# Performance work log

Hardware: AMD Instinct MI355X
Metric: run time of the kernel (lower is better)

## Reference

```python
import jax, jax.numpy as jnp
import numpy as np

N_TASKS = 32
D = 2097152  # flattened gradient dim
MAX_ITER = 250
STOP_CRIT = 1e-6
EPS = 1e-8


def setup_inputs() -> dict:
    key = jax.random.key(0)
    vecs = jax.random.normal(key, (N_TASKS, D), dtype=jnp.float32)
    return {"vecs": vecs}


def _line_solver(v11, v12, v22):
    # min-norm point on the segment between two vectors (vectorized / scalar)
    g = (v22 - v12) / (v11 + v22 - 2.0 * v12 + EPS)
    c = v22 + g * (v12 - v22)
    gamma = jnp.where(v12 >= v22, 0.0, g)
    gamma = jnp.where(v12 >= v11, 1.0, gamma)
    cost = jnp.where(v12 >= v22, v22, c)
    cost = jnp.where(v12 >= v11, v11, cost)
    return gamma, cost


def _planar_init(G, n):
    iu_np, ju_np = np.triu_indices(n, 1)
    iu = jnp.asarray(iu_np)
    ju = jnp.asarray(ju_np)
    vivj = G[iu, ju]
    vivi = G[iu, iu]
    vjvj = G[ju, ju]
    gamma, cost = _line_solver(vivi, vivj, vjvj)
    off = jnp.argmin(cost)
    sol = jnp.zeros(n, dtype=G.dtype)
    sol = sol.at[iu[off]].set(gamma[off]).at[ju[off]].set(1.0 - gamma[off])
    return sol


def _proj_simplex(gamma, i_grid):
    s = jnp.sort(gamma)[::-1]  # descending
    tmp_max = (jnp.cumsum(s) - 1.0) / i_grid
    cond = tmp_max[:-1] > s[1:]
    first = jnp.argmax(cond)  # index of first True (0 if none)
    tmax = jnp.where(jnp.any(cond), tmp_max[:-1][first], tmp_max[-1])
    return jnp.maximum(gamma - tmax, 0.0)


def _next_point(cur, grad, n, i_grid):
    proj = grad - jnp.sum(grad) / n
    neg = proj < 0
    pos = proj > 0
    tm1 = jnp.where(neg, -cur / jnp.where(neg, proj, 1.0), jnp.inf)
    tm2 = jnp.where(pos, (1.0 - cur) / jnp.where(pos, proj, 1.0), jnp.inf)
    m1 = jnp.min(jnp.where(tm1 > 1e-7, tm1, jnp.inf))
    t = jnp.where(jnp.isfinite(m1), m1, 1.0)
    m2 = jnp.min(jnp.where(tm2 > 1e-7, tm2, jnp.inf))
    t = jnp.minimum(t, m2)  # no-op if m2 is inf
    nxt = proj * t + cur
    return _proj_simplex(nxt, i_grid)


def reference(vecs):
    n = vecs.shape[0]
    G = vecs @ vecs.T  # [n, n] grammian; only memory-heavy step
    sol0 = _planar_init(G, n)
    i_grid = jnp.arange(n, dtype=G.dtype) + 1.0
    n_f = jnp.asarray(n, dtype=G.dtype)

    def body(carry, _):
        sol, done = carry
        grad_dir = -(G @ sol)
        newp = _next_point(sol, grad_dir, n_f, i_grid)
        Gs = G @ sol
        Gn = G @ newp
        v11 = sol @ Gs
        v12 = sol @ Gn
        v22 = newp @ Gn
        gamma, _ = _line_solver(v11, v12, v22)
        new_sol = gamma * sol + (1.0 - gamma) * newp
        stop = jnp.sum(jnp.abs(new_sol - sol)) < STOP_CRIT
        nd = done | stop
        # original returns the OLD sol_vec when change < stop_crit
        out = jnp.where(nd, sol, new_sol)
        return (out, nd), None

    (sol, _), _ = jax.lax.scan(body, (sol0, jnp.array(False)), None, length=MAX_ITER)
    return sol
```

## Files before the change

kernel.cpp:

```cpp
#include <hip/hip_runtime.h>

#define NT 32
#define EPSF 1e-8f

#define TILE_COLS 64
#define COL_PITCH 36
#define GR_THREADS 256
#define WAVES_PB 4
#define TILES_PW 16

__global__ __launch_bounds__(GR_THREADS, 2)
void gram_kernel(const float* __restrict__ vecs, double* __restrict__ Gd, int D)
{
    __shared__ float tile[WAVES_PB][TILE_COLS * COL_PITCH];
    __shared__ float Gpart[NT * NT];

    const int tid  = threadIdx.x;
    const int wave = tid >> 6;
    const int lane = tid & 63;

    for (int e = tid; e < NT * NT; e += GR_THREADS) Gpart[e] = 0.0f;
    __syncthreads();

    const int cj = lane >> 4;
    const int p  = lane & 15;
    const int pi = p >> 2;
    const int pk = p & 3;

    const int lrow = lane >> 4;
    const int lcol = (lane & 15) << 2;

    float acc[8][8];
#pragma unroll
    for (int r = 0; r < 8; r++)
#pragma unroll
        for (int c = 0; c < 8; c++) acc[r][c] = 0.0f;

    float* my = tile[wave];
    const long colbase0 = (long)blockIdx.x * (WAVES_PB * TILES_PW * TILE_COLS)
                        + (long)wave * (TILES_PW * TILE_COLS);

    float4 pre[8];
#pragma unroll
    for (int rr = 0; rr < 8; rr++) {
        const int row = (rr << 2) + lrow;
        pre[rr] = *(const float4*)(vecs + (long)row * D + colbase0 + lcol);
    }

    for (int t = 0; t < TILES_PW; t++) {
        __threadfence_block();
#pragma unroll
        for (int rr = 0; rr < 8; rr++) {
            const int row = (rr << 2) + lrow;
            my[(lcol + 0) * COL_PITCH + row] = pre[rr].x;
            my[(lcol + 1) * COL_PITCH + row] = pre[rr].y;
            my[(lcol + 2) * COL_PITCH + row] = pre[rr].z;
            my[(lcol + 3) * COL_PITCH + row] = pre[rr].w;
        }
        __threadfence_block();
        if (t + 1 < TILES_PW) {
            const long cb = colbase0 + (long)(t + 1) * TILE_COLS;
#pragma unroll
            for (int rr = 0; rr < 8; rr++) {
                const int row = (rr << 2) + lrow;
                pre[rr] = *(const float4*)(vecs + (long)row * D + cb + lcol);
            }
        }
#pragma unroll
        for (int jt = 0; jt < 16; jt++) {
            const int j = (jt << 2) + cj;
            const float* col = my + j * COL_PITCH;
            const float4 a0 = *(const float4*)(col + 8 * pi);
            const float4 a1 = *(const float4*)(col + 8 * pi + 4);
            const float4 b0 = *(const float4*)(col + 8 * pk);
            const float4 b1 = *(const float4*)(col + 8 * pk + 4);
            const float a[8] = {a0.x, a0.y, a0.z, a0.w, a1.x, a1.y, a1.z, a1.w};
            const float b[8] = {b0.x, b0.y, b0.z, b0.w, b1.x, b1.y, b1.z, b1.w};
#pragma unroll
            for (int r = 0; r < 8; r++)
#pragma unroll
                for (int c = 0; c < 8; c++)
                    acc[r][c] = fmaf(a[r], b[c], acc[r][c]);
        }
    }

#pragma unroll
    for (int r = 0; r < 8; r++)
#pragma unroll
        for (int c = 0; c < 8; c++) {
            float v = acc[r][c];
            v += __shfl_xor(v, 16);
            v += __shfl_xor(v, 32);
            if (lane < 16)
                atomicAdd(&Gpart[(8 * pi + r) * NT + (8 * pk + c)], v);
        }
    __syncthreads();
    for (int e = tid; e < NT * NT; e += GR_THREADS)
        atomicAdd(&Gd[e], (double)Gpart[e]);
}

__device__ __forceinline__ float bsum32(float v) {
#pragma unroll
    for (int m = 1; m < 32; m <<= 1) v += __shfl_xor(v, m);
    return v;
}
__device__ __forceinline__ float bmin32(float v) {
#pragma unroll
    for (int m = 1; m < 32; m <<= 1) v = fminf(v, __shfl_xor(v, m));
    return v;
}

__global__ __launch_bounds__(64)
void solver_kernel(const double* __restrict__ Gd, float* __restrict__ out)
{
    __shared__ float Gsh[NT * 33];
    const int lane = threadIdx.x;

    for (int t2 = 0; t2 < 16; t2++) {
        int e = t2 * 64 + lane;
        Gsh[(e >> 5) * 33 + (e & 31)] = (float)Gd[e];
    }
    __syncthreads();

    float Grow[NT];
#pragma unroll
    for (int k = 0; k < NT; k++)
        Grow[k] = (lane < NT) ? Gsh[lane * 33 + k] : 0.0f;

    float bestCost = INFINITY, bestGamma = 0.0f;
    int bestEnc = 0x7FFFFFFF;
    for (int a = 0; a < NT - 1; a++) {
        int b = a + 1 + lane;
        if (b < NT) {
            float v11 = Gsh[a * 33 + a];
            float v12 = Gsh[a * 33 + b];
            float v22 = Gsh[b * 33 + b];
            float g = (v22 - v12) / (v11 + v22 - 2.0f * v12 + EPSF);
            float c = v22 + g * (v12 - v22);
            float gamma = (v12 >= v22) ? 0.0f : g;
            float cost  = (v12 >= v22) ? v22 : c;
            if (v12 >= v11) { gamma = 1.0f; cost = v11; }
            int enc = a * NT + b;
            if (cost < bestCost) { bestCost = cost; bestEnc = enc; bestGamma = gamma; }
        }
    }
#pragma unroll
    for (int m = 1; m < 64; m <<= 1) {
        float oc = __shfl_xor(bestCost, m);
        int   oe = __shfl_xor(bestEnc, m);
        float og = __shfl_xor(bestGamma, m);
        if (oc < bestCost || (oc == bestCost && oe < bestEnc)) {
            bestCost = oc; bestEnc = oe; bestGamma = og;
        }
    }
    const int bi = bestEnc >> 5, bj = bestEnc & 31;

    float sol = 0.0f;
    if (lane == bi) sol = bestGamma;
    if (lane == bj) sol = 1.0f - bestGamma;

    for (int it = 0; it < 250; it++) {
        float s0 = 0, s1 = 0, s2 = 0, s3 = 0;
#pragma unroll
        for (int k = 0; k < NT; k += 4) {
            s0 = fmaf(Grow[k + 0], __shfl(sol, k + 0), s0);
            s1 = fmaf(Grow[k + 1], __shfl(sol, k + 1), s1);
            s2 = fmaf(Grow[k + 2], __shfl(sol, k + 2), s2);
            s3 = fmaf(Grow[k + 3], __shfl(sol, k + 3), s3);
        }
        float Gsol = (s0 + s1) + (s2 + s3);

        float grad = -Gsol;
        float proj = grad - bsum32(grad) * 0.03125f;

        float tm1 = (proj < 0.0f) ? (-sol / proj) : INFINITY;
        float tm2 = (proj > 0.0f) ? ((1.0f - sol) / proj) : INFINITY;
        float m1 = bmin32((tm1 > 1e-7f) ? tm1 : INFINITY);
        float m2 = bmin32((tm2 > 1e-7f) ? tm2 : INFINITY);
        float t = __builtin_isinf(m1) ? 1.0f : m1;
        t = fminf(t, m2);
        float nxt = fmaf(proj, t, sol);

        float s = nxt;
#pragma unroll
        for (int k = 2; k <= 32; k <<= 1)
#pragma unroll
            for (int j = k >> 1; j >= 1; j >>= 1) {
                float pp = __shfl_xor(s, j);
                bool descSeg = (lane & k) == 0;
                bool lower = (lane & j) == 0;
                float mn = fminf(s, pp), mx = fmaxf(s, pp);
                s = (descSeg == lower) ? mx : mn;
            }
        float cs = s;
#pragma unroll
        for (int d = 1; d < 32; d <<= 1) {
            float pp = __shfl_up(cs, d, 32);
            if ((lane & 31) >= d) cs += pp;
        }
        float tmpm = (cs - 1.0f) / (float)((lane & 31) + 1);
        float snext = __shfl_down(s, 1, 32);
        bool cond = ((lane & 31) < 31) && (tmpm > snext);
        unsigned long long bal = __ballot(cond ? 1 : 0) & 0x7FFFFFFFull;
        float tmax;
        if (bal != 0ULL) {
            int first = __builtin_ctzll(bal);
            tmax = __shfl(tmpm, first);
        } else {
            tmax = __shfl(tmpm, 31);
        }
        float newp = fmaxf(nxt - tmax, 0.0f);
        if (lane >= NT) newp = 0.0f;

        float n0 = 0, n1 = 0, n2 = 0, n3 = 0;
#pragma unroll
        for (int k = 0; k < NT; k += 4) {
            n0 = fmaf(Grow[k + 0], __shfl(newp, k + 0), n0);
            n1 = fmaf(Grow[k + 1], __shfl(newp, k + 1), n1);
            n2 = fmaf(Grow[k + 2], __shfl(newp, k + 2), n2);
            n3 = fmaf(Grow[k + 3], __shfl(newp, k + 3), n3);
        }
        float Gn = (n0 + n1) + (n2 + n3);

        float v11 = bsum32(sol * Gsol);
        float v12 = bsum32(sol * Gn);
        float v22 = bsum32(newp * Gn);

        float g = (v22 - v12) / (v11 + v22 - 2.0f * v12 + EPSF);
        float gamma = (v12 >= v22) ? 0.0f : g;
        gamma = (v12 >= v11) ? 1.0f : gamma;

        float new_sol = gamma * sol + (1.0f - gamma) * newp;
        float diff = bsum32(fabsf(new_sol - sol));
        diff = __shfl(diff, 0);
        if (diff < 1e-6f) break;
        sol = new_sol;
    }
    if (lane < NT) out[lane] = sol;
}

extern "C" void kernel_launch(void* const* d_in, const int* in_sizes, int n_in,
                              void* d_out, int out_size, void* d_ws, size_t ws_size,
                              hipStream_t stream) {
    const float* vecs = (const float*)d_in[0];
    float* out = (float*)d_out;
    double* Gd = (double*)d_ws;
    const int D = in_sizes[0] / NT;

    hipMemsetAsync(Gd, 0, NT * NT * sizeof(double), stream);

    const int cols_per_block = WAVES_PB * TILES_PW * TILE_COLS;
    const int grid = D / cols_per_block;
    gram_kernel<<<grid, GR_THREADS, 0, stream>>>(vecs, Gd, D);
    solver_kernel<<<1, 64, 0, stream>>>(Gd, out);
}
```

Before: 430.1 us.

## Swizzle Gram tile layout, halve tiles per wave, use DPP/readlane in solver

The Gram kernel now loads one column per lane with scalar loads and stores rows into an XOR-swizzled 32-wide shared tile instead of a padded transpose. Tiles per wave drop to 8 and the occupancy hint rises to 4 blocks per CU, doubling the grid. The serial solver swaps ds_bpermute-based shuffles for DPP row ops, ds_swizzle and readlane to shorten the per-iteration latency chain. The risks are more register pressure from the 32-float prefetch array, scalar global loads that may coalesce worse, and subtle cross-row DPP correctness in the scans.

```diff
diff --git a/kernel.cpp b/kernel.cpp
--- a/kernel.cpp
+++ b/kernel.cpp
@@ -4,15 +4,14 @@
 #define EPSF 1e-8f
 
 #define TILE_COLS 64
-#define COL_PITCH 36
 #define GR_THREADS 256
 #define WAVES_PB 4
-#define TILES_PW 16
-
-__global__ __launch_bounds__(GR_THREADS, 2)
+#define TILES_PW 8
+
+__global__ __launch_bounds__(GR_THREADS, 4)
 void gram_kernel(const float* __restrict__ vecs, double* __restrict__ Gd, int D)
 {
-    __shared__ float tile[WAVES_PB][TILE_COLS * COL_PITCH];
+    __shared__ __align__(16) float tile[WAVES_PB][TILE_COLS * 32];
     __shared__ float Gpart[NT * NT];
 
     const int tid  = threadIdx.x;
@@ -22,13 +21,12 @@
     for (int e = tid; e < NT * NT; e += GR_THREADS) Gpart[e] = 0.0f;
     __syncthreads();
 
+    float* my = tile[wave];
+    const int swz = lane & 7;
+
     const int cj = lane >> 4;
-    const int p  = lane & 15;
-    const int pi = p >> 2;
-    const int pk = p & 3;
-
-    const int lrow = lane >> 4;
-    const int lcol = (lane & 15) << 2;
+    const int pi = (lane >> 2) & 3;
+    const int pk = lane & 3;
 
     float acc[8][8];
 #pragma unroll
@@ -36,44 +34,34 @@
 #pragma unroll
         for (int c = 0; c < 8; c++) acc[r][c] = 0.0f;
 
-    float* my = tile[wave];
-    const long colbase0 = (long)blockIdx.x * (WAVES_PB * TILES_PW * TILE_COLS)
-                        + (long)wave * (TILES_PW * TILE_COLS);
-
-    float4 pre[8];
-#pragma unroll
-    for (int rr = 0; rr < 8; rr++) {
-        const int row = (rr << 2) + lrow;
-        pre[rr] = *(const float4*)(vecs + (long)row * D + colbase0 + lcol);
-    }
+    const long base0 = (long)blockIdx.x * (WAVES_PB * TILES_PW * TILE_COLS)
+                     + (long)wave * (TILES_PW * TILE_COLS) + lane;
+
+    float pre[32];
+#pragma unroll
+    for (int r = 0; r < 32; r++) pre[r] = vecs[(long)r * D + base0];
 
     for (int t = 0; t < TILES_PW; t++) {
-        __threadfence_block();
-#pragma unroll
-        for (int rr = 0; rr < 8; rr++) {
-            const int row = (rr << 2) + lrow;
-            my[(lcol + 0) * COL_PITCH + row] = pre[rr].x;
-            my[(lcol + 1) * COL_PITCH + row] = pre[rr].y;
-            my[(lcol + 2) * COL_PITCH + row] = pre[rr].z;
-            my[(lcol + 3) * COL_PITCH + row] = pre[rr].w;
-        }
-        __threadfence_block();
+#pragma unroll
+        for (int rg = 0; rg < 8; rg++) {
+            float4 w = make_float4(pre[4 * rg], pre[4 * rg + 1],
+                                   pre[4 * rg + 2], pre[4 * rg + 3]);
+            *(float4*)(my + lane * 32 + (((rg ^ swz)) << 2)) = w;
+        }
         if (t + 1 < TILES_PW) {
-            const long cb = colbase0 + (long)(t + 1) * TILE_COLS;
-#pragma unroll
-            for (int rr = 0; rr < 8; rr++) {
-                const int row = (rr << 2) + lrow;
-                pre[rr] = *(const float4*)(vecs + (long)row * D + cb + lcol);
-            }
+            const long b = base0 + (long)(t + 1) * TILE_COLS;
+#pragma unroll
+            for (int r = 0; r < 32; r++) pre[r] = vecs[(long)r * D + b];
         }
 #pragma unroll
         for (int jt = 0; jt < 16; jt++) {
             const int j = (jt << 2) + cj;
-            const float* col = my + j * COL_PITCH;
-            const float4 a0 = *(const float4*)(col + 8 * pi);
-            const float4 a1 = *(const float4*)(col + 8 * pi + 4);
-            const float4 b0 = *(const float4*)(col + 8 * pk);
-            const float4 b1 = *(const float4*)(col + 8 * pk + 4);
+            const float* col = my + j * 32;
+            const int js = j & 7;
+            const float4 a0 = *(const float4*)(col + (((2 * pi) ^ js) << 2));
+            const float4 a1 = *(const float4*)(col + (((2 * pi + 1) ^ js) << 2));
+            const float4 b0 = *(const float4*)(col + (((2 * pk) ^ js) << 2));
+            const float4 b1 = *(const float4*)(col + (((2 * pk + 1) ^ js) << 2));
             const float a[8] = {a0.x, a0.y, a0.z, a0.w, a1.x, a1.y, a1.z, a1.w};
             const float b[8] = {b0.x, b0.y, b0.z, b0.w, b1.x, b1.y, b1.z, b1.w};
 #pragma unroll
@@ -99,15 +87,47 @@
         atomicAdd(&Gd[e], (double)Gpart[e]);
 }
 
-__device__ __forceinline__ float bsum32(float v) {
-#pragma unroll
-    for (int m = 1; m < 32; m <<= 1) v += __shfl_xor(v, m);
-    return v;
-}
-__device__ __forceinline__ float bmin32(float v) {
-#pragma unroll
-    for (int m = 1; m < 32; m <<= 1) v = fminf(v, __shfl_xor(v, m));
-    return v;
+template<int CTRL>
+__device__ __forceinline__ float dpp0(float x) {
+    return __int_as_float(__builtin_amdgcn_update_dpp(
+        0, __float_as_int(x), CTRL, 0xF, 0xF, true));
+}
+template<int CTRL>
+__device__ __forceinline__ float dppk(float oldv, float x) {
+    return __int_as_float(__builtin_amdgcn_update_dpp(
+        __float_as_int(oldv), __float_as_int(x), CTRL, 0xF, 0xF, false));
+}
+__device__ __forceinline__ float rdlane(float x, int l) {
+    return __int_as_float(__builtin_amdgcn_readlane(__float_as_int(x), l));
+}
+
+__device__ __forceinline__ float bsum32u(float v) {
+    v += dpp0<0x111>(v);
+    v += dpp0<0x112>(v);
+    v += dpp0<0x114>(v);
+    v += dpp0<0x118>(v);
+    return rdlane(v, 15) + rdlane(v, 31);
+}
+__device__ __forceinline__ float bmin32u(float v) {
+    v = fminf(v, dppk<0x111>(v, v));
+    v = fminf(v, dppk<0x112>(v, v));
+    v = fminf(v, dppk<0x114>(v, v));
+    v = fminf(v, dppk<0x118>(v, v));
+    return fminf(rdlane(v, 15), rdlane(v, 31));
+}
+
+template<int J>
+__device__ __forceinline__ float partner(float x) {
+    if constexpr (J == 1)
+        return dpp0<0xB1>(x);
+    else if constexpr (J == 2)
+        return dpp0<0x4E>(x);
+    else if constexpr (J == 4)
+        return __int_as_float(__builtin_amdgcn_ds_swizzle(__float_as_int(x), 0x101F));
+    else if constexpr (J == 8)
+        return __int_as_float(__builtin_amdgcn_ds_swizzle(__float_as_int(x), 0x201F));
+    else
+        return __int_as_float(__builtin_amdgcn_ds_swizzle(__float_as_int(x), 0x401F));
 }
 
 __global__ __launch_bounds__(64)
@@ -163,51 +183,58 @@
         float s0 = 0, s1 = 0, s2 = 0, s3 = 0;
 #pragma unroll
         for (int k = 0; k < NT; k += 4) {
-            s0 = fmaf(Grow[k + 0], __shfl(sol, k + 0), s0);
-            s1 = fmaf(Grow[k + 1], __shfl(sol, k + 1), s1);
-            s2 = fmaf(Grow[k + 2], __shfl(sol, k + 2), s2);
-            s3 = fmaf(Grow[k + 3], __shfl(sol, k + 3), s3);
+            s0 = fmaf(Grow[k + 0], rdlane(sol, k + 0), s0);
+            s1 = fmaf(Grow[k + 1], rdlane(sol, k + 1), s1);
+            s2 = fmaf(Grow[k + 2], rdlane(sol, k + 2), s2);
+            s3 = fmaf(Grow[k + 3], rdlane(sol, k + 3), s3);
         }
         float Gsol = (s0 + s1) + (s2 + s3);
 
         float grad = -Gsol;
-        float proj = grad - bsum32(grad) * 0.03125f;
+        float proj = grad - bsum32u(grad) * 0.03125f;
 
         float tm1 = (proj < 0.0f) ? (-sol / proj) : INFINITY;
         float tm2 = (proj > 0.0f) ? ((1.0f - sol) / proj) : INFINITY;
-        float m1 = bmin32((tm1 > 1e-7f) ? tm1 : INFINITY);
-        float m2 = bmin32((tm2 > 1e-7f) ? tm2 : INFINITY);
+        float m1 = bmin32u((tm1 > 1e-7f) ? tm1 : INFINITY);
+        float m2 = bmin32u((tm2 > 1e-7f) ? tm2 : INFINITY);
         float t = __builtin_isinf(m1) ? 1.0f : m1;
         t = fminf(t, m2);
         float nxt = fmaf(proj, t, sol);
 
         float s = nxt;
-#pragma unroll
-        for (int k = 2; k <= 32; k <<= 1)
-#pragma unroll
-            for (int j = k >> 1; j >= 1; j >>= 1) {
-                float pp = __shfl_xor(s, j);
-                bool descSeg = (lane & k) == 0;
-                bool lower = (lane & j) == 0;
-                float mn = fminf(s, pp), mx = fmaxf(s, pp);
-                s = (descSeg == lower) ? mx : mn;
-            }
+#define BSTAGE(KK, JJ) { \
+        float pp = partner<JJ>(s); \
+        bool descSeg = (lane & KK) == 0; \
+        bool lower = (lane & JJ) == 0; \
+        float mn = fminf(s, pp), mx = fmaxf(s, pp); \
+        s = (descSeg == lower) ? mx : mn; }
+        BSTAGE(2, 1)
+        BSTAGE(4, 2)  BSTAGE(4, 1)
+        BSTAGE(8, 4)  BSTAGE(8, 2)  BSTAGE(8, 1)
+        BSTAGE(16, 8) BSTAGE(16, 4) BSTAGE(16, 2) BSTAGE(16, 1)
+        BSTAGE(32, 16) BSTAGE(32, 8) BSTAGE(32, 4) BSTAGE(32, 2) BSTAGE(32, 1)
+#undef BSTAGE
+
         float cs = s;
-#pragma unroll
-        for (int d = 1; d < 32; d <<= 1) {
-            float pp = __shfl_up(cs, d, 32);
-            if ((lane & 31) >= d) cs += pp;
-        }
+        cs += dpp0<0x111>(cs);
+        cs += dpp0<0x112>(cs);
+        cs += dpp0<0x114>(cs);
+        cs += dpp0<0x118>(cs);
+        float bc = dppk<0x142>(0.0f, cs);
+        cs += (lane & 16) ? bc : 0.0f;
+
         float tmpm = (cs - 1.0f) / (float)((lane & 31) + 1);
-        float snext = __shfl_down(s, 1, 32);
+        float snext = dppk<0x101>(s, s);
+        float s16 = rdlane(s, 16);
+        if ((lane & 31) == 15) snext = s16;
         bool cond = ((lane & 31) < 31) && (tmpm > snext);
         unsigned long long bal = __ballot(cond ? 1 : 0) & 0x7FFFFFFFull;
         float tmax;
         if (bal != 0ULL) {
             int first = __builtin_ctzll(bal);
-            tmax = __shfl(tmpm, first);
+            tmax = rdlane(tmpm, first);
         } else {
-            tmax = __shfl(tmpm, 31);
+            tmax = rdlane(tmpm, 31);
         }
         float newp = fmaxf(nxt - tmax, 0.0f);
         if (lane >= NT) newp = 0.0f;
@@ -215,24 +242,23 @@
         float n0 = 0, n1 = 0, n2 = 0, n3 = 0;
 #pragma unroll
         for (int k = 0; k < NT; k += 4) {
-            n0 = fmaf(Grow[k + 0], __shfl(newp, k + 0), n0);
-            n1 = fmaf(Grow[k + 1], __shfl(newp, k + 1), n1);
-            n2 = fmaf(Grow[k + 2], __shfl(newp, k + 2), n2);
-            n3 = fmaf(Grow[k + 3], __shfl(newp, k + 3), n3);
+            n0 = fmaf(Grow[k + 0], rdlane(newp, k + 0), n0);
+            n1 = fmaf(Grow[k + 1], rdlane(newp, k + 1), n1);
+            n2 = fmaf(Grow[k + 2], rdlane(newp, k + 2), n2);
+            n3 = fmaf(Grow[k + 3], rdlane(newp, k + 3), n3);
         }
         float Gn = (n0 + n1) + (n2 + n3);
 
-        float v11 = bsum32(sol * Gsol);
-        float v12 = bsum32(sol * Gn);
-        float v22 = bsum32(newp * Gn);
+        float v11 = bsum32u(sol * Gsol);
+        float v12 = bsum32u(sol * Gn);
+        float v22 = bsum32u(newp * Gn);
 
         float g = (v22 - v12) / (v11 + v22 - 2.0f * v12 + EPSF);
         float gamma = (v12 >= v22) ? 0.0f : g;
         gamma = (v12 >= v11) ? 1.0f : gamma;
 
         float new_sol = gamma * sol + (1.0f - gamma) * newp;
-        float diff = bsum32(fabsf(new_sol - sol));
-        diff = __shfl(diff, 0);
+        float diff = bsum32u(fabsf(new_sol - sol));
         if (diff < 1e-6f) break;
         sol = new_sol;
     }
```

Measured after the change: 629.2 us. 46.3% more time.
